# Performance work log

Measured on AMD Instinct MI355X. Metric: run time of the kernel, lower is better.

The kernel has to match this reference:

```python
import jax, jax.numpy as jnp
import numpy as np

N = 50000
R = 8
E = 100000
D_IN = 768
D_H = 256
LN_EPS = 1e-5


def _layer_norm(h, g, b):
    mu = jnp.mean(h, axis=-1, keepdims=True)
    var = jnp.mean((h - mu) ** 2, axis=-1, keepdims=True)
    return (h - mu) * jax.lax.rsqrt(var + LN_EPS) * g + b


def _rgcn_layer(x, node_w, edge_src, edge_tgt, W_rel, W_self_w, W_self_b, ln_g, ln_b):
    # x: [N, d_in]; edge_src/edge_tgt: [R, E]; W_rel: [R, d_in, d_out]
    n = x.shape[0]
    out = x @ W_self_w + W_self_b  # self loop
    for r in range(W_rel.shape[0]):  # fixed, small relation count
        src = edge_src[r]
        tgt = edge_tgt[r]
        feats = x[src] * node_w[src][:, None]          # gather + nuclearity scale, [E, d_in]
        msg = feats @ W_rel[r]                          # per-relation linear, [E, d_out]
        agg = jax.ops.segment_sum(msg, tgt, num_segments=n)                 # scatter_add
        cnt = jax.ops.segment_sum(jnp.ones(src.shape[0], x.dtype), tgt, num_segments=n)
        out = out + agg / jnp.clip(cnt, 1.0)[:, None]  # mean over relation neighbors
    return _layer_norm(jax.nn.relu(out), ln_g, ln_b)   # dropout = identity (eval)


def setup_inputs() -> dict:
    key = jax.random.key(0)
    ks = jax.random.split(key, 10)
    x = jax.random.normal(ks[0], (N, D_IN), dtype=jnp.float32)
    node_weights = jax.random.uniform(ks[1], (N,), dtype=jnp.float32)
    edge_src = jax.random.randint(ks[2], (R, E), 0, N, dtype=jnp.int32)
    edge_tgt = jax.random.randint(ks[3], (R, E), 0, N, dtype=jnp.int32)
    W_rel0 = jax.random.normal(ks[4], (R, D_IN, D_H), dtype=jnp.float32) / np.sqrt(D_IN)
    W_self0_w = jax.random.normal(ks[5], (D_IN, D_H), dtype=jnp.float32) / np.sqrt(D_IN)
    W_self0_b = jnp.zeros((D_H,), jnp.float32)
    W_rel1 = jax.random.normal(ks[6], (R, D_H, D_H), dtype=jnp.float32) / np.sqrt(D_H)
    W_self1_w = jax.random.normal(ks[7], (D_H, D_H), dtype=jnp.float32) / np.sqrt(D_H)
    W_self1_b = jnp.zeros((D_H,), jnp.float32)
    ones = jnp.ones((D_H,), jnp.float32)
    zeros = jnp.zeros((D_H,), jnp.float32)
    return {
        "x": x, "node_weights": node_weights,
        "edge_src": edge_src, "edge_tgt": edge_tgt,
        "W_rel0": W_rel0, "W_self0_w": W_self0_w, "W_self0_b": W_self0_b,
        "ln0_g": ones, "ln0_b": zeros,
        "W_rel1": W_rel1, "W_self1_w": W_self1_w, "W_self1_b": W_self1_b,
        "ln1_g": ones, "ln1_b": zeros,
    }


def reference(x, node_weights, edge_src, edge_tgt,
              W_rel0, W_self0_w, W_self0_b, ln0_g, ln0_b,
              W_rel1, W_self1_w, W_self1_b, ln1_g, ln1_b):
    h = _rgcn_layer(x, node_weights, edge_src, edge_tgt,
                    W_rel0, W_self0_w, W_self0_b, ln0_g, ln0_b)
    h = _rgcn_layer(h, node_weights, edge_src, edge_tgt,
                    W_rel1, W_self1_w, W_self1_b, ln1_g, ln1_b)
    return h  # [N, 256]
```

## Files before the change

### kernel.cpp

```cpp
#include <hip/hip_runtime.h>
#include <stdint.h>

#define N_NODES 50000
#define M_PAD   50048
#define R_REL   8
#define E_EDGES 100000
#define D_IN    768
#define D_H     256
#define N_CAT   2304
#define LN_EPS  1e-5f

#define TILES_N 18
#define TILES_M 391
#define T_TOT   (TILES_N * TILES_M)
#define T_PER_XCD ((T_TOT + 7) / 8)
#define NCHUNK  49

typedef __attribute__((ext_vector_type(8))) __bf16        bf16x8;
typedef __attribute__((ext_vector_type(4))) float         f32x4;
typedef __attribute__((ext_vector_type(8))) unsigned short u16x8;
typedef __attribute__((ext_vector_type(4))) unsigned short u16x4;
typedef __attribute__((ext_vector_type(4))) int            i32x4;

__device__ __forceinline__ float bf2f(unsigned short u) {
  union { float f; uint32_t i; } c; c.i = ((uint32_t)u) << 16; return c.f;
}
__device__ __forceinline__ unsigned short f2bf(float f) {
  uint32_t x = __float_as_uint(f);
  uint32_t r = (x + 0x7fffu + ((x >> 16) & 1u)) >> 16;
  return (unsigned short)r;
}

__device__ __forceinline__ void gload_lds16(const void* g, uint32_t lds_off) {
  __builtin_amdgcn_global_load_lds(
      (const __attribute__((address_space(1))) void*)(uintptr_t)g,
      (__attribute__((address_space(3))) void*)(uintptr_t)lds_off, 16, 0, 0);
}

__global__ void k_deg(const int* __restrict__ tgt, int* __restrict__ deg) {
  int e = blockIdx.x * 256 + threadIdx.x;
  if (e >= R_REL * E_EDGES) return;
  int r = e / E_EDGES;
  atomicAdd(&deg[r * N_NODES + tgt[e]], 1);
}

__global__ __launch_bounds__(256)
void k_scan1(const int* __restrict__ deg, int* __restrict__ rowptr,
             int* __restrict__ bsum) {
  __shared__ int wtot[4];
  const int r = blockIdx.y, chunk = blockIdx.x, tid = threadIdx.x;
  const int wave = tid >> 6, lane = tid & 63;
  const int i0 = chunk * 1024 + tid * 4;
  int v0 = 0, v1 = 0, v2 = 0, v3 = 0;
  const int* d = deg + r * N_NODES;
  if (chunk != NCHUNK - 1) {
    i32x4 v = *(const i32x4*)(d + i0);
    v0 = v[0]; v1 = v[1]; v2 = v[2]; v3 = v[3];
  } else {
    if (i0 + 0 < N_NODES) v0 = d[i0 + 0];
    if (i0 + 1 < N_NODES) v1 = d[i0 + 1];
    if (i0 + 2 < N_NODES) v2 = d[i0 + 2];
    if (i0 + 3 < N_NODES) v3 = d[i0 + 3];
  }
  const int tsum = v0 + v1 + v2 + v3;
  int inc = tsum;
#pragma unroll
  for (int off = 1; off < 64; off <<= 1) {
    int t = __shfl_up(inc, off, 64);
    if (lane >= off) inc += t;
  }
  if (lane == 63) wtot[wave] = inc;
  __syncthreads();
  int woff = 0;
#pragma unroll
  for (int w = 0; w < 4; ++w) woff += (w < wave) ? wtot[w] : 0;
  int excl = woff + inc - tsum;
  int* rp = rowptr + r * (N_NODES + 1);
  if (i0 + 0 < N_NODES) rp[i0 + 0] = excl;
  if (i0 + 1 < N_NODES) rp[i0 + 1] = excl + v0;
  if (i0 + 2 < N_NODES) rp[i0 + 2] = excl + v0 + v1;
  if (i0 + 3 < N_NODES) rp[i0 + 3] = excl + v0 + v1 + v2;
  if (tid == 0) bsum[r * NCHUNK + chunk] = wtot[0] + wtot[1] + wtot[2] + wtot[3];
}

__global__ __launch_bounds__(512)
void k_scan2(const int* __restrict__ bsum, int* __restrict__ chunkoff,
             int* __restrict__ rowptr) {
  const int r = threadIdx.x >> 6, lane = threadIdx.x & 63;
  int v = (lane < NCHUNK) ? bsum[r * NCHUNK + lane] : 0;
  int inc = v;
#pragma unroll
  for (int off = 1; off < 64; off <<= 1) {
    int t = __shfl_up(inc, off, 64);
    if (lane >= off) inc += t;
  }
  if (lane < NCHUNK) chunkoff[r * NCHUNK + lane] = inc - v;
  if (lane == NCHUNK - 1) rowptr[r * (N_NODES + 1) + N_NODES] = inc;
}

__global__ __launch_bounds__(256)
void k_scan3(const int* __restrict__ chunkoff, int* __restrict__ rowptr) {
  const int r = blockIdx.y, chunk = blockIdx.x;
  if (chunk == 0) return;
  const int off = chunkoff[r * NCHUNK + chunk];
  const int i0 = chunk * 1024 + threadIdx.x * 4;
  int* rp = rowptr + r * (N_NODES + 1);
#pragma unroll
  for (int j = 0; j < 4; ++j)
    if (i0 + j < N_NODES) rp[i0 + j] += off;
}

__global__ void k_fill(const int* __restrict__ src, const int* __restrict__ tgt,
                       const float* __restrict__ nw, const int* __restrict__ rowptr,
                       int* __restrict__ cursor, int2* __restrict__ e2) {
  int e = blockIdx.x * 256 + threadIdx.x;
  if (e >= R_REL * E_EDGES) return;
  int r = e / E_EDGES;
  int t = tgt[e], s = src[e];
  int pos = atomicAdd(&cursor[r * N_NODES + t], 1);
  int slot = r * E_EDGES + rowptr[r * (N_NODES + 1) + t] + pos;
  e2[slot] = make_int2(s, __float_as_int(nw[s]));
}

__global__ void k_cvt_x(const float* __restrict__ x, unsigned short* __restrict__ xb) {
  const size_t i = ((size_t)blockIdx.x * 256 + threadIdx.x) * 4;
  if (i >= (size_t)N_NODES * D_IN) return;
  const f32x4 v = *(const f32x4*)(x + i);
  u16x4 o = { f2bf(v[0]), f2bf(v[1]), f2bf(v[2]), f2bf(v[3]) };
  *(u16x4*)(xb + i) = o;
}

__global__ void k_cvt_w(const float* __restrict__ Ws, const float* __restrict__ Wr,
                        unsigned short* __restrict__ Wt, int K) {
  int idx = blockIdx.x * 256 + threadIdx.x;
  if (idx >= N_CAT * K) return;
  int n = idx / K, k = idx - n * K;
  float v = (n < 256) ? Ws[k * 256 + n]
                      : Wr[(size_t)((n - 256) >> 8) * K * 256 + k * 256 + (n & 255)];
  Wt[idx] = f2bf(v);
}

__global__ __launch_bounds__(256, 2)
void k_gemm(const unsigned short* __restrict__ A, const unsigned short* __restrict__ Bt,
            unsigned short* __restrict__ C, int K) {
  const int tile = (blockIdx.x & 7) * T_PER_XCD + (blockIdx.x >> 3);
  if (tile >= T_TOT) return;
  const int tileM = (tile / TILES_N) * 128;
  const int tileN = (tile % TILES_N) * 128;

  __shared__ __align__(16) char smem[32768];
  const int tid  = threadIdx.x;
  const int wave = tid >> 6, lane = tid & 63;
  const int wm = (wave >> 1) * 64, wn = (wave & 1) * 64;

  f32x4 acc[4][4] = {};

  const int srow = wave * 32 + (lane >> 2);
  const int kchunk = ((lane & 3) - ((lane >> 2) & 3)) & 3;
  const unsigned short* gA = A  + (size_t)(tileM + srow) * K + kchunk * 8;
  const unsigned short* gB = Bt + (size_t)(tileN + srow) * K + kchunk * 8;
  const uint32_t ldsA = (uint32_t)(uintptr_t)smem;
  const uint32_t ldsB = ldsA + 8192;
  const uint32_t lA0 = ldsA + (wave * 32) * 64;
  const uint32_t lB0 = ldsB + (wave * 32) * 64;
  const size_t rowstep = (size_t)16 * K;

  const int slot = (((lane >> 4) + (lane & 3)) & 3) * 16;
  const char* pA = smem        + (wm + (lane & 15)) * 64 + slot;
  const char* pB = smem + 8192 + (wn + (lane & 15)) * 64 + slot;

  const int nk = K >> 5;
  for (int kt = 0; kt < nk; ++kt) {
    const int koff = kt * 32;
    __syncthreads();
    gload_lds16(gA + koff,           lA0);
    gload_lds16(gA + rowstep + koff, lA0 + 16 * 64);
    gload_lds16(gB + koff,           lB0);
    gload_lds16(gB + rowstep + koff, lB0 + 16 * 64);
    __syncthreads();
    bf16x8 af[4], bfr[4];
#pragma unroll
    for (int i = 0; i < 4; ++i) af[i]  = *(const bf16x8*)(pA + i * 1024);
#pragma unroll
    for (int j = 0; j < 4; ++j) bfr[j] = *(const bf16x8*)(pB + j * 1024);
#pragma unroll
    for (int i = 0; i < 4; ++i)
#pragma unroll
      for (int j = 0; j < 4; ++j)
        acc[i][j] = __builtin_amdgcn_mfma_f32_16x16x32_bf16(af[i], bfr[j], acc[i][j], 0, 0, 0);
  }

  __syncthreads();
  unsigned short* st = (unsigned short*)smem + wave * 4096;
  const int rq = (lane >> 4) * 4, cq = lane & 15;
#pragma unroll
  for (int i = 0; i < 4; ++i)
#pragma unroll
    for (int j = 0; j < 4; ++j)
#pragma unroll
      for (int p = 0; p < 4; ++p)
        st[(i * 16 + rq + p) * 64 + j * 16 + cq] = f2bf(acc[i][j][p]);
  __syncthreads();
#pragma unroll
  for (int pass = 0; pass < 8; ++pass) {
    const int row = pass * 8 + (lane >> 3);
    u16x8 v = *(const u16x8*)(st + row * 64 + (lane & 7) * 8);
    size_t off = (size_t)(tileM + wm + row) * N_CAT + tileN + wn + (lane & 7) * 8;
    *(u16x8*)(C + off) = v;
  }
}

template <int FINAL>
__global__ __launch_bounds__(256)
void k_gather_ln(const unsigned short* __restrict__ Y, const int* __restrict__ rowptr,
                 const int2* __restrict__ e2, const float* __restrict__ bias,
                 const float* __restrict__ g, const float* __restrict__ bln,
                 void* __restrict__ out) {
  const int wave = threadIdx.x >> 6, lane = threadIdx.x & 63;
  const int t = blockIdx.x * 4 + wave;
  if (t >= N_NODES) return;
  const int c0 = lane * 4;

  float a0, a1, a2, a3;
  {
    u16x4 sv = *(const u16x4*)(Y + (size_t)t * N_CAT + c0);
    a0 = bf2f(sv[0]) + bias[c0 + 0];
    a1 = bf2f(sv[1]) + bias[c0 + 1];
    a2 = bf2f(sv[2]) + bias[c0 + 2];
    a3 = bf2f(sv[3]) + bias[c0 + 3];
  }
#pragma unroll
  for (int r = 0; r < R_REL; ++r) {
    const int rp0 = rowptr[r * (N_NODES + 1) + t];
    const int rp1 = rowptr[r * (N_NODES + 1) + t + 1];
    if (rp0 == rp1) continue;
    float r0 = 0, r1 = 0, r2 = 0, r3 = 0;
    float q0 = 0, q1 = 0, q2 = 0, q3 = 0;
    const int base = r * E_EDGES;
    const size_t colr = (size_t)(1 + r) * 256 + c0;
    int idx = rp0;
    for (; idx + 2 <= rp1; idx += 2) {
      const int2 p0 = e2[base + idx];
      const int2 p1 = e2[base + idx + 1];
      const float w0 = __int_as_float(p0.y);
      const float w1 = __int_as_float(p1.y);
      u16x4 v0 = *(const u16x4*)(Y + (size_t)p0.x * N_CAT + colr);
      u16x4 v1 = *(const u16x4*)(Y + (size_t)p1.x * N_CAT + colr);
      r0 += w0 * bf2f(v0[0]); r1 += w0 * bf2f(v0[1]);
      r2 += w0 * bf2f(v0[2]); r3 += w0 * bf2f(v0[3]);
      q0 += w1 * bf2f(v1[0]); q1 += w1 * bf2f(v1[1]);
      q2 += w1 * bf2f(v1[2]); q3 += w1 * bf2f(v1[3]);
    }
    if (idx < rp1) {
      const int2 p0 = e2[base + idx];
      const float w0 = __int_as_float(p0.y);
      u16x4 v0 = *(const u16x4*)(Y + (size_t)p0.x * N_CAT + colr);
      r0 += w0 * bf2f(v0[0]); r1 += w0 * bf2f(v0[1]);
      r2 += w0 * bf2f(v0[2]); r3 += w0 * bf2f(v0[3]);
    }
    const float inv = 1.0f / (float)(rp1 - rp0);
    a0 += inv * (r0 + q0); a1 += inv * (r1 + q1);
    a2 += inv * (r2 + q2); a3 += inv * (r3 + q3);
  }
  a0 = fmaxf(a0, 0.f); a1 = fmaxf(a1, 0.f); a2 = fmaxf(a2, 0.f); a3 = fmaxf(a3, 0.f);

  float s1 = a0 + a1 + a2 + a3;
#pragma unroll
  for (int off = 32; off > 0; off >>= 1) s1 += __shfl_xor(s1, off, 64);
  const float mu = s1 * (1.f / 256.f);
  const float d0 = a0 - mu, d1 = a1 - mu, d2 = a2 - mu, d3 = a3 - mu;
  float s2 = d0 * d0 + d1 * d1 + d2 * d2 + d3 * d3;
#pragma unroll
  for (int off = 32; off > 0; off >>= 1) s2 += __shfl_xor(s2, off, 64);
  const float rs = rsqrtf(s2 * (1.f / 256.f) + LN_EPS);
  const float o0 = d0 * rs * g[c0 + 0] + bln[c0 + 0];
  const float o1 = d1 * rs * g[c0 + 1] + bln[c0 + 1];
  const float o2 = d2 * rs * g[c0 + 2] + bln[c0 + 2];
  const float o3 = d3 * rs * g[c0 + 3] + bln[c0 + 3];
  if (FINAL) {
    f32x4 o = { o0, o1, o2, o3 };
    *(f32x4*)((float*)out + (size_t)t * 256 + c0) = o;
  } else {
    u16x4 o = { f2bf(o0), f2bf(o1), f2bf(o2), f2bf(o3) };
    *(u16x4*)((unsigned short*)out + (size_t)t * 256 + c0) = o;
  }
}

extern "C" void kernel_launch(void* const* d_in, const int* in_sizes, int n_in,
                              void* d_out, int out_size, void* d_ws, size_t ws_size,
                              hipStream_t stream) {
  (void)in_sizes; (void)n_in; (void)out_size; (void)ws_size;
  const float* x   = (const float*)d_in[0];
  const float* nw  = (const float*)d_in[1];
  const int*   esrc = (const int*)d_in[2];
  const int*   etgt = (const int*)d_in[3];
  const float* Wr0 = (const float*)d_in[4];
  const float* Ws0 = (const float*)d_in[5];
  const float* Wb0 = (const float*)d_in[6];
  const float* g0  = (const float*)d_in[7];
  const float* b0  = (const float*)d_in[8];
  const float* Wr1 = (const float*)d_in[9];
  const float* Ws1 = (const float*)d_in[10];
  const float* Wb1 = (const float*)d_in[11];
  const float* g1  = (const float*)d_in[12];
  const float* b1  = (const float*)d_in[13];

  char* p = (char*)d_ws;
  auto carve = [&](size_t bytes) {
    char* q = p;
    p += (bytes + 511) & ~(size_t)511;
    return q;
  };
  unsigned short* Y   = (unsigned short*)carve((size_t)M_PAD * N_CAT * 2);
  unsigned short* xb  = (unsigned short*)carve((size_t)M_PAD * D_IN * 2);
  unsigned short* h   = (unsigned short*)carve((size_t)M_PAD * D_H * 2);
  unsigned short* Wt0 = (unsigned short*)carve((size_t)N_CAT * D_IN * 2);
  unsigned short* Wt1 = (unsigned short*)carve((size_t)N_CAT * D_H * 2);
  int*   deg     = (int*)carve((size_t)R_REL * N_NODES * 4);
  int*   cursor  = (int*)carve((size_t)R_REL * N_NODES * 4);
  int*   rowptr  = (int*)carve((size_t)R_REL * (N_NODES + 1) * 4);
  int*   bsum    = (int*)carve((size_t)R_REL * NCHUNK * 4);
  int*   chunkoff= (int*)carve((size_t)R_REL * NCHUNK * 4);
  int2*  e2      = (int2*)carve((size_t)R_REL * E_EDGES * 8);

  hipMemsetAsync(deg, 0, (size_t)R_REL * N_NODES * 4, stream);
  hipMemsetAsync(cursor, 0, (size_t)R_REL * N_NODES * 4, stream);
  k_deg<<<(R_REL * E_EDGES + 255) / 256, 256, 0, stream>>>(etgt, deg);
  k_scan1<<<dim3(NCHUNK, R_REL), 256, 0, stream>>>(deg, rowptr, bsum);
  k_scan2<<<1, 512, 0, stream>>>(bsum, chunkoff, rowptr);
  k_scan3<<<dim3(NCHUNK, R_REL), 256, 0, stream>>>(chunkoff, rowptr);
  k_fill<<<(R_REL * E_EDGES + 255) / 256, 256, 0, stream>>>(esrc, etgt, nw, rowptr,
                                                            cursor, e2);
  k_cvt_x<<<(N_NODES * D_IN / 4 + 255) / 256, 256, 0, stream>>>(x, xb);
  k_cvt_w<<<(N_CAT * D_IN + 255) / 256, 256, 0, stream>>>(Ws0, Wr0, Wt0, D_IN);
  k_cvt_w<<<(N_CAT * D_H + 255) / 256, 256, 0, stream>>>(Ws1, Wr1, Wt1, D_H);

  const int nblk = 8 * T_PER_XCD;
  k_gemm<<<nblk, 256, 0, stream>>>(xb, Wt0, Y, D_IN);
  k_gather_ln<0><<<N_NODES / 4, 256, 0, stream>>>(Y, rowptr, e2, Wb0, g0, b0, h);
  k_gemm<<<nblk, 256, 0, stream>>>(h, Wt1, Y, D_H);
  k_gather_ln<1><<<N_NODES / 4, 256, 0, stream>>>(Y, rowptr, e2, Wb1, g1, b1, d_out);
}
```

Measured before the change: 894.7 us.

## Merge per-relation CSR into padded per-node edge list and widen GEMM K-tile

Builds one CSR over target nodes covering all relations. Each node's edge count is padded to a multiple of 4, and the 1/deg mean normalisation and relation index are folded into each edge record, so the gather loop runs one unrolled-by-4 pass instead of eight per-relation loops. The GEMM now loads a 64-wide K slab per iteration with an XOR swizzle, halving barrier pairs, and pads the epilogue staging stride to reduce LDS bank conflicts. The cost is a memset of a larger padded edge buffer, and packing the source node in 16 bits breaks for node ids of 65536 or more.

```diff
diff --git a/kernel.cpp b/kernel.cpp
--- a/kernel.cpp
+++ b/kernel.cpp
@@ -15,6 +15,8 @@
 #define T_TOT   (TILES_N * TILES_M)
 #define T_PER_XCD ((T_TOT + 7) / 8)
 #define NCHUNK  49
+#define EP_STRIDE 68
+#define E_PAD_MAX 960000
 
 typedef __attribute__((ext_vector_type(8))) __bf16        bf16x8;
 typedef __attribute__((ext_vector_type(4))) float         f32x4;
@@ -44,15 +46,24 @@
   atomicAdd(&deg[r * N_NODES + tgt[e]], 1);
 }
 
+__global__ void k_ndeg(const int* __restrict__ deg, int* __restrict__ pdeg) {
+  int t = blockIdx.x * 256 + threadIdx.x;
+  if (t >= N_NODES) return;
+  int s = 0;
+#pragma unroll
+  for (int r = 0; r < R_REL; ++r) s += deg[r * N_NODES + t];
+  pdeg[t] = (s + 3) & ~3;
+}
+
 __global__ __launch_bounds__(256)
 void k_scan1(const int* __restrict__ deg, int* __restrict__ rowptr,
              int* __restrict__ bsum) {
   __shared__ int wtot[4];
-  const int r = blockIdx.y, chunk = blockIdx.x, tid = threadIdx.x;
+  const int chunk = blockIdx.x, tid = threadIdx.x;
   const int wave = tid >> 6, lane = tid & 63;
   const int i0 = chunk * 1024 + tid * 4;
   int v0 = 0, v1 = 0, v2 = 0, v3 = 0;
-  const int* d = deg + r * N_NODES;
+  const int* d = deg;
   if (chunk != NCHUNK - 1) {
     i32x4 v = *(const i32x4*)(d + i0);
     v0 = v[0]; v1 = v[1]; v2 = v[2]; v3 = v[3];
@@ -75,51 +86,58 @@
 #pragma unroll
   for (int w = 0; w < 4; ++w) woff += (w < wave) ? wtot[w] : 0;
   int excl = woff + inc - tsum;
-  int* rp = rowptr + r * (N_NODES + 1);
+  int* rp = rowptr;
   if (i0 + 0 < N_NODES) rp[i0 + 0] = excl;
   if (i0 + 1 < N_NODES) rp[i0 + 1] = excl + v0;
   if (i0 + 2 < N_NODES) rp[i0 + 2] = excl + v0 + v1;
   if (i0 + 3 < N_NODES) rp[i0 + 3] = excl + v0 + v1 + v2;
-  if (tid == 0) bsum[r * NCHUNK + chunk] = wtot[0] + wtot[1] + wtot[2] + wtot[3];
-}
-
-__global__ __launch_bounds__(512)
+  if (tid == 0) bsum[chunk] = wtot[0] + wtot[1] + wtot[2] + wtot[3];
+}
+
+__global__ __launch_bounds__(64)
 void k_scan2(const int* __restrict__ bsum, int* __restrict__ chunkoff,
              int* __restrict__ rowptr) {
-  const int r = threadIdx.x >> 6, lane = threadIdx.x & 63;
-  int v = (lane < NCHUNK) ? bsum[r * NCHUNK + lane] : 0;
+  const int lane = threadIdx.x & 63;
+  int v = (lane < NCHUNK) ? bsum[lane] : 0;
   int inc = v;
 #pragma unroll
   for (int off = 1; off < 64; off <<= 1) {
     int t = __shfl_up(inc, off, 64);
     if (lane >= off) inc += t;
   }
-  if (lane < NCHUNK) chunkoff[r * NCHUNK + lane] = inc - v;
-  if (lane == NCHUNK - 1) rowptr[r * (N_NODES + 1) + N_NODES] = inc;
+  if (lane < NCHUNK) chunkoff[lane] = inc - v;
+  if (lane == NCHUNK - 1) rowptr[N_NODES] = inc;
 }
 
 __global__ __launch_bounds__(256)
 void k_scan3(const int* __restrict__ chunkoff, int* __restrict__ rowptr) {
-  const int r = blockIdx.y, chunk = blockIdx.x;
+  const int chunk = blockIdx.x;
   if (chunk == 0) return;
-  const int off = chunkoff[r * NCHUNK + chunk];
+  const int off = chunkoff[chunk];
   const int i0 = chunk * 1024 + threadIdx.x * 4;
-  int* rp = rowptr + r * (N_NODES + 1);
 #pragma unroll
   for (int j = 0; j < 4; ++j)
-    if (i0 + j < N_NODES) rp[i0 + j] += off;
+    if (i0 + j < N_NODES) rowptr[i0 + j] += off;
+}
+
+__global__ void k_prep(const int* __restrict__ nodeptr, int2* __restrict__ scN) {
+  int t = blockIdx.x * 256 + threadIdx.x;
+  if (t >= N_NODES) return;
+  scN[t] = make_int2(nodeptr[t], nodeptr[t + 1] - nodeptr[t]);
 }
 
 __global__ void k_fill(const int* __restrict__ src, const int* __restrict__ tgt,
-                       const float* __restrict__ nw, const int* __restrict__ rowptr,
-                       int* __restrict__ cursor, int2* __restrict__ e2) {
+                       const float* __restrict__ nw, const int* __restrict__ nodeptr,
+                       const int* __restrict__ deg, int* __restrict__ cursor,
+                       int2* __restrict__ e2) {
   int e = blockIdx.x * 256 + threadIdx.x;
   if (e >= R_REL * E_EDGES) return;
   int r = e / E_EDGES;
   int t = tgt[e], s = src[e];
-  int pos = atomicAdd(&cursor[r * N_NODES + t], 1);
-  int slot = r * E_EDGES + rowptr[r * (N_NODES + 1) + t] + pos;
-  e2[slot] = make_int2(s, __float_as_int(nw[s]));
+  int pos = atomicAdd(&cursor[t], 1);
+  int slot = nodeptr[t] + pos;
+  float w = nw[s] / (float)deg[r * N_NODES + t];
+  e2[slot] = make_int2(s | (r << 16), __float_as_int(w));
 }
 
 __global__ void k_cvt_x(const float* __restrict__ x, unsigned short* __restrict__ xb) {
@@ -148,50 +166,55 @@
   const int tileM = (tile / TILES_N) * 128;
   const int tileN = (tile % TILES_N) * 128;
 
-  __shared__ __align__(16) char smem[32768];
+  __shared__ __align__(16) char smem[34816];
   const int tid  = threadIdx.x;
   const int wave = tid >> 6, lane = tid & 63;
   const int wm = (wave >> 1) * 64, wn = (wave & 1) * 64;
 
   f32x4 acc[4][4] = {};
 
-  const int srow = wave * 32 + (lane >> 2);
-  const int kchunk = ((lane & 3) - ((lane >> 2) & 3)) & 3;
-  const unsigned short* gA = A  + (size_t)(tileM + srow) * K + kchunk * 8;
-  const unsigned short* gB = Bt + (size_t)(tileN + srow) * K + kchunk * 8;
+  const int rl = lane >> 3, sl8 = lane & 7;
+  const int cch = sl8 ^ rl;
+  const int srow = wave * 8 + rl;
+  const unsigned short* gA = A  + (size_t)(tileM + srow) * K + cch * 8;
+  const unsigned short* gB = Bt + (size_t)(tileN + srow) * K + cch * 8;
   const uint32_t ldsA = (uint32_t)(uintptr_t)smem;
-  const uint32_t ldsB = ldsA + 8192;
-  const uint32_t lA0 = ldsA + (wave * 32) * 64;
-  const uint32_t lB0 = ldsB + (wave * 32) * 64;
-  const size_t rowstep = (size_t)16 * K;
-
-  const int slot = (((lane >> 4) + (lane & 3)) & 3) * 16;
-  const char* pA = smem        + (wm + (lane & 15)) * 64 + slot;
-  const char* pB = smem + 8192 + (wn + (lane & 15)) * 64 + slot;
-
-  const int nk = K >> 5;
+  const uint32_t ldsB = ldsA + 16384;
+  const uint32_t lA0 = ldsA + (wave * 8) * 128;
+  const uint32_t lB0 = ldsB + (wave * 8) * 128;
+
+  const char* pAb = smem         + (wm + (lane & 15)) * 128;
+  const char* pBb = smem + 16384 + (wn + (lane & 15)) * 128;
+  const int fph = lane >> 4, x7 = lane & 7;
+
+  const int nk = K >> 6;
   for (int kt = 0; kt < nk; ++kt) {
-    const int koff = kt * 32;
+    const size_t koff = (size_t)kt * 64;
     __syncthreads();
-    gload_lds16(gA + koff,           lA0);
-    gload_lds16(gA + rowstep + koff, lA0 + 16 * 64);
-    gload_lds16(gB + koff,           lB0);
-    gload_lds16(gB + rowstep + koff, lB0 + 16 * 64);
+#pragma unroll
+    for (int j = 0; j < 4; ++j) {
+      gload_lds16(gA + (size_t)j * 32 * K + koff, lA0 + j * 4096);
+      gload_lds16(gB + (size_t)j * 32 * K + koff, lB0 + j * 4096);
+    }
     __syncthreads();
-    bf16x8 af[4], bfr[4];
-#pragma unroll
-    for (int i = 0; i < 4; ++i) af[i]  = *(const bf16x8*)(pA + i * 1024);
-#pragma unroll
-    for (int j = 0; j < 4; ++j) bfr[j] = *(const bf16x8*)(pB + j * 1024);
-#pragma unroll
-    for (int i = 0; i < 4; ++i)
-#pragma unroll
-      for (int j = 0; j < 4; ++j)
-        acc[i][j] = __builtin_amdgcn_mfma_f32_16x16x32_bf16(af[i], bfr[j], acc[i][j], 0, 0, 0);
+#pragma unroll
+    for (int kk = 0; kk < 2; ++kk) {
+      const int sA = ((kk * 4 + fph) ^ x7) * 16;
+      bf16x8 af[4], bfr[4];
+#pragma unroll
+      for (int i = 0; i < 4; ++i) af[i]  = *(const bf16x8*)(pAb + i * 2048 + sA);
+#pragma unroll
+      for (int j = 0; j < 4; ++j) bfr[j] = *(const bf16x8*)(pBb + j * 2048 + sA);
+#pragma unroll
+      for (int i = 0; i < 4; ++i)
+#pragma unroll
+        for (int j = 0; j < 4; ++j)
+          acc[i][j] = __builtin_amdgcn_mfma_f32_16x16x32_bf16(af[i], bfr[j], acc[i][j], 0, 0, 0);
+    }
   }
 
   __syncthreads();
-  unsigned short* st = (unsigned short*)smem + wave * 4096;
+  unsigned short* st = (unsigned short*)smem + wave * (64 * EP_STRIDE);
   const int rq = (lane >> 4) * 4, cq = lane & 15;
 #pragma unroll
   for (int i = 0; i < 4; ++i)
@@ -199,12 +222,14 @@
     for (int j = 0; j < 4; ++j)
 #pragma unroll
       for (int p = 0; p < 4; ++p)
-        st[(i * 16 + rq + p) * 64 + j * 16 + cq] = f2bf(acc[i][j][p]);
-  __syncthreads();
+        st[(i * 16 + rq + p) * EP_STRIDE + j * 16 + cq] = f2bf(acc[i][j][p]);
 #pragma unroll
   for (int pass = 0; pass < 8; ++pass) {
     const int row = pass * 8 + (lane >> 3);
-    u16x8 v = *(const u16x8*)(st + row * 64 + (lane & 7) * 8);
+    const unsigned short* rp_ = st + row * EP_STRIDE + (lane & 7) * 8;
+    u16x4 lo = *(const u16x4*)(rp_);
+    u16x4 hi = *(const u16x4*)(rp_ + 4);
+    u16x8 v = { lo[0], lo[1], lo[2], lo[3], hi[0], hi[1], hi[2], hi[3] };
     size_t off = (size_t)(tileM + wm + row) * N_CAT + tileN + wn + (lane & 7) * 8;
     *(u16x8*)(C + off) = v;
   }
@@ -212,7 +237,7 @@
 
 template <int FINAL>
 __global__ __launch_bounds__(256)
-void k_gather_ln(const unsigned short* __restrict__ Y, const int* __restrict__ rowptr,
+void k_gather_ln(const unsigned short* __restrict__ Y, const int2* __restrict__ scN,
                  const int2* __restrict__ e2, const float* __restrict__ bias,
                  const float* __restrict__ g, const float* __restrict__ bln,
                  void* __restrict__ out) {
@@ -224,59 +249,54 @@
   float a0, a1, a2, a3;
   {
     u16x4 sv = *(const u16x4*)(Y + (size_t)t * N_CAT + c0);
-    a0 = bf2f(sv[0]) + bias[c0 + 0];
-    a1 = bf2f(sv[1]) + bias[c0 + 1];
-    a2 = bf2f(sv[2]) + bias[c0 + 2];
-    a3 = bf2f(sv[3]) + bias[c0 + 3];
-  }
-#pragma unroll
-  for (int r = 0; r < R_REL; ++r) {
-    const int rp0 = rowptr[r * (N_NODES + 1) + t];
-    const int rp1 = rowptr[r * (N_NODES + 1) + t + 1];
-    if (rp0 == rp1) continue;
-    float r0 = 0, r1 = 0, r2 = 0, r3 = 0;
-    float q0 = 0, q1 = 0, q2 = 0, q3 = 0;
-    const int base = r * E_EDGES;
-    const size_t colr = (size_t)(1 + r) * 256 + c0;
-    int idx = rp0;
-    for (; idx + 2 <= rp1; idx += 2) {
-      const int2 p0 = e2[base + idx];
-      const int2 p1 = e2[base + idx + 1];
-      const float w0 = __int_as_float(p0.y);
-      const float w1 = __int_as_float(p1.y);
-      u16x4 v0 = *(const u16x4*)(Y + (size_t)p0.x * N_CAT + colr);
-      u16x4 v1 = *(const u16x4*)(Y + (size_t)p1.x * N_CAT + colr);
-      r0 += w0 * bf2f(v0[0]); r1 += w0 * bf2f(v0[1]);
-      r2 += w0 * bf2f(v0[2]); r3 += w0 * bf2f(v0[3]);
-      q0 += w1 * bf2f(v1[0]); q1 += w1 * bf2f(v1[1]);
-      q2 += w1 * bf2f(v1[2]); q3 += w1 * bf2f(v1[3]);
-    }
-    if (idx < rp1) {
-      const int2 p0 = e2[base + idx];
-      const float w0 = __int_as_float(p0.y);
-      u16x4 v0 = *(const u16x4*)(Y + (size_t)p0.x * N_CAT + colr);
-      r0 += w0 * bf2f(v0[0]); r1 += w0 * bf2f(v0[1]);
-      r2 += w0 * bf2f(v0[2]); r3 += w0 * bf2f(v0[3]);
-    }
-    const float inv = 1.0f / (float)(rp1 - rp0);
-    a0 += inv * (r0 + q0); a1 += inv * (r1 + q1);
-    a2 += inv * (r2 + q2); a3 += inv * (r3 + q3);
-  }
+    f32x4 bb = *(const f32x4*)(bias + c0);
+    a0 = bf2f(sv[0]) + bb[0];
+    a1 = bf2f(sv[1]) + bb[1];
+    a2 = bf2f(sv[2]) + bb[2];
+    a3 = bf2f(sv[3]) + bb[3];
+  }
+
+  const int2 s = scN[t];
+  const int2* ep = e2 + s.x;
+  for (int idx = 0; idx < s.y; idx += 4) {
+    const int2 p0 = ep[idx + 0];
+    const int2 p1 = ep[idx + 1];
+    const int2 p2 = ep[idx + 2];
+    const int2 p3 = ep[idx + 3];
+    const unsigned short* y0 = Y + (size_t)(p0.x & 0xFFFF) * N_CAT + (((p0.x >> 16) + 1) << 8) + c0;
+    const unsigned short* y1 = Y + (size_t)(p1.x & 0xFFFF) * N_CAT + (((p1.x >> 16) + 1) << 8) + c0;
+    const unsigned short* y2 = Y + (size_t)(p2.x & 0xFFFF) * N_CAT + (((p2.x >> 16) + 1) << 8) + c0;
+    const unsigned short* y3 = Y + (size_t)(p3.x & 0xFFFF) * N_CAT + (((p3.x >> 16) + 1) << 8) + c0;
+    u16x4 v0 = *(const u16x4*)y0;
+    u16x4 v1 = *(const u16x4*)y1;
+    u16x4 v2 = *(const u16x4*)y2;
+    u16x4 v3 = *(const u16x4*)y3;
+    const float w0 = __int_as_float(p0.y), w1 = __int_as_float(p1.y);
+    const float w2 = __int_as_float(p2.y), w3 = __int_as_float(p3.y);
+    a0 += w0 * bf2f(v0[0]) + w1 * bf2f(v1[0]) + w2 * bf2f(v2[0]) + w3 * bf2f(v3[0]);
+    a1 += w0 * bf2f(v0[1]) + w1 * bf2f(v1[1]) + w2 * bf2f(v2[1]) + w3 * bf2f(v3[1]);
+    a2 += w0 * bf2f(v0[2]) + w1 * bf2f(v1[2]) + w2 * bf2f(v2[2]) + w3 * bf2f(v3[2]);
+    a3 += w0 * bf2f(v0[3]) + w1 * bf2f(v1[3]) + w2 * bf2f(v2[3]) + w3 * bf2f(v3[3]);
+  }
+
   a0 = fmaxf(a0, 0.f); a1 = fmaxf(a1, 0.f); a2 = fmaxf(a2, 0.f); a3 = fmaxf(a3, 0.f);
 
-  float s1 = a0 + a1 + a2 + a3;
+  float s1 = (a0 + a1) + (a2 + a3);
 #pragma unroll
   for (int off = 32; off > 0; off >>= 1) s1 += __shfl_xor(s1, off, 64);
   const float mu = s1 * (1.f / 256.f);
   const float d0 = a0 - mu, d1 = a1 - mu, d2 = a2 - mu, d3 = a3 - mu;
-  float s2 = d0 * d0 + d1 * d1 + d2 * d2 + d3 * d3;
+  float s2 = (d0 * d0 + d1 * d1) + (d2 * d2 + d3 * d3);
 #pragma unroll
   for (int off = 32; off > 0; off >>= 1) s2 += __shfl_xor(s2, off, 64);
   const float rs = rsqrtf(s2 * (1.f / 256.f) + LN_EPS);
-  const float o0 = d0 * rs * g[c0 + 0] + bln[c0 + 0];
-  const float o1 = d1 * rs * g[c0 + 1] + bln[c0 + 1];
-  const float o2 = d2 * rs * g[c0 + 2] + bln[c0 + 2];
-  const float o3 = d3 * rs * g[c0 + 3] + bln[c0 + 3];
+
+  f32x4 gg = *(const f32x4*)(g + c0);
+  f32x4 ll = *(const f32x4*)(bln + c0);
+  const float o0 = d0 * rs * gg[0] + ll[0];
+  const float o1 = d1 * rs * gg[1] + ll[1];
+  const float o2 = d2 * rs * gg[2] + ll[2];
+  const float o3 = d3 * rs * gg[3] + ll[3];
   if (FINAL) {
     f32x4 o = { o0, o1, o2, o3 };
     *(f32x4*)((float*)out + (size_t)t * 256 + c0) = o;
@@ -317,27 +337,32 @@
   unsigned short* Wt0 = (unsigned short*)carve((size_t)N_CAT * D_IN * 2);
   unsigned short* Wt1 = (unsigned short*)carve((size_t)N_CAT * D_H * 2);
   int*   deg     = (int*)carve((size_t)R_REL * N_NODES * 4);
-  int*   cursor  = (int*)carve((size_t)R_REL * N_NODES * 4);
-  int*   rowptr  = (int*)carve((size_t)R_REL * (N_NODES + 1) * 4);
-  int*   bsum    = (int*)carve((size_t)R_REL * NCHUNK * 4);
-  int*   chunkoff= (int*)carve((size_t)R_REL * NCHUNK * 4);
-  int2*  e2      = (int2*)carve((size_t)R_REL * E_EDGES * 8);
+  int*   pdeg    = (int*)carve((size_t)N_NODES * 4);
+  int*   cursor  = (int*)carve((size_t)N_NODES * 4);
+  int*   nodeptr = (int*)carve((size_t)(N_NODES + 1) * 4);
+  int*   bsum    = (int*)carve((size_t)NCHUNK * 4);
+  int*   chunkoff= (int*)carve((size_t)NCHUNK * 4);
+  int2*  e2      = (int2*)carve((size_t)E_PAD_MAX * 8);
+  int2*  scN     = (int2*)carve((size_t)N_NODES * 8);
 
   hipMemsetAsync(deg, 0, (size_t)R_REL * N_NODES * 4, stream);
-  hipMemsetAsync(cursor, 0, (size_t)R_REL * N_NODES * 4, stream);
+  hipMemsetAsync(cursor, 0, (size_t)N_NODES * 4, stream);
+  hipMemsetAsync(e2, 0, (size_t)E_PAD_MAX * 8, stream);
   k_deg<<<(R_REL * E_EDGES + 255) / 256, 256, 0, stream>>>(etgt, deg);
-  k_scan1<<<dim3(NCHUNK, R_REL), 256, 0, stream>>>(deg, rowptr, bsum);
-  k_scan2<<<1, 512, 0, stream>>>(bsum, chunkoff, rowptr);
-  k_scan3<<<dim3(NCHUNK, R_REL), 256, 0, stream>>>(chunkoff, rowptr);
-  k_fill<<<(R_REL * E_EDGES + 255) / 256, 256, 0, stream>>>(esrc, etgt, nw, rowptr,
-                                                            cursor, e2);
+  k_ndeg<<<(N_NODES + 255) / 256, 256, 0, stream>>>(deg, pdeg);
+  k_scan1<<<NCHUNK, 256, 0, stream>>>(pdeg, nodeptr, bsum);
+  k_scan2<<<1, 64, 0, stream>>>(bsum, chunkoff, nodeptr);
+  k_scan3<<<NCHUNK, 256, 0, stream>>>(chunkoff, nodeptr);
+  k_prep<<<(N_NODES + 255) / 256, 256, 0, stream>>>(nodeptr, scN);
+  k_fill<<<(R_REL * E_EDGES + 255) / 256, 256, 0, stream>>>(esrc, etgt, nw, nodeptr,
+                                                            deg, cursor, e2);
   k_cvt_x<<<(N_NODES * D_IN / 4 + 255) / 256, 256, 0, stream>>>(x, xb);
   k_cvt_w<<<(N_CAT * D_IN + 255) / 256, 256, 0, stream>>>(Ws0, Wr0, Wt0, D_IN);
   k_cvt_w<<<(N_CAT * D_H + 255) / 256, 256, 0, stream>>>(Ws1, Wr1, Wt1, D_H);
 
   const int nblk = 8 * T_PER_XCD;
   k_gemm<<<nblk, 256, 0, stream>>>(xb, Wt0, Y, D_IN);
-  k_gather_ln<0><<<N_NODES / 4, 256, 0, stream>>>(Y, rowptr, e2, Wb0, g0, b0, h);
+  k_gather_ln<0><<<N_NODES / 4, 256, 0, stream>>>(Y, scN, e2, Wb0, g0, b0, h);
   k_gemm<<<nblk, 256, 0, stream>>>(h, Wt1, Y, D_H);
-  k_gather_ln<1><<<N_NODES / 4, 256, 0, stream>>>(Y, rowptr, e2, Wb1, g1, b1, d_out);
-}
+  k_gather_ln<1><<<N_NODES / 4, 256, 0, stream>>>(Y, scN, e2, Wb1, g1, b1, d_out);
+}
```

Result: faster. 797.8 us (-10.8%).
